# Performance work log

Measured on AMD Instinct MI355X. Metric: run time of the kernel, lower is better.

## Reference

```python
import jax, jax.numpy as jnp
import numpy as np

N, E, G = 20000, 160000, 64
IN_FULL, X_START, X_END = 16, 4, 10
H, OUT, RH, NE, K = 512, 512, 128, 4, 2
NL = 3               # GraphConv layers per expert
SPS, STEMP = 0.3, 1.0  # size_prior_strength, size_temperature


def setup_inputs() -> dict:
    key = jax.random.key(0)
    ks = jax.random.split(key, 10)
    def w(k, shape, fan):
        return jax.random.normal(k, shape, jnp.float32) / np.float32(np.sqrt(fan))
    return dict(
        x=jax.random.normal(ks[0], (N, IN_FULL), jnp.float32),
        edge_index=jax.random.randint(ks[1], (2, E), 0, N),
        batch=jnp.sort(jax.random.randint(ks[2], (N,), 0, G)),
        num_graphs=G,
        enc_W1=w(ks[3], (X_END - X_START, H), X_END - X_START), enc_b1=jnp.zeros((H,), jnp.float32),
        enc_W2=w(ks[4], (H, H), H), enc_b2=jnp.zeros((H,), jnp.float32),
        r_W1=w(ks[5], (H + 2, RH), H + 2), r_b1=jnp.zeros((RH,), jnp.float32),
        ln_g=jnp.ones((RH,), jnp.float32), ln_b=jnp.zeros((RH,), jnp.float32),
        r_W2=w(ks[6], (RH, NE), RH), r_b2=jnp.zeros((NE,), jnp.float32),
        size_centers=jnp.linspace(0.0, 1.0, NE).astype(jnp.float32),
        W_rel=w(ks[7], (NE, NL, H, H), H),       # GraphConv lin_rel weights (stacked)
        b_rel=jnp.zeros((NE, NL, H), jnp.float32),
        W_root=w(ks[8], (NE, NL, H, H), H),      # GraphConv lin_root weights (no bias)
    )


def reference(x, edge_index, batch, num_graphs, enc_W1, enc_b1, enc_W2, enc_b2,
              r_W1, r_b1, ln_g, ln_b, r_W2, r_b2, size_centers, W_rel, b_rel, W_root):
    src, dst = edge_index[0], edge_index[1]
    # encoder: Linear -> ReLU -> Linear on sliced node features
    h = jax.nn.relu(x[:, X_START:X_END] @ enc_W1 + enc_b1) @ enc_W2 + enc_b2
    # per-graph size features (log_nodes_edges mode)
    nodes = jnp.maximum(jax.ops.segment_sum(jnp.ones((N,), x.dtype), batch, num_segments=num_graphs), 1.0)
    edges = jax.ops.segment_sum(jnp.ones((E,), x.dtype), batch[src], num_segments=num_graphs)
    log_n, log_e = jnp.log(nodes), jnp.log1p(edges)
    f = jnp.stack([log_n, log_e], axis=-1)
    f = (f - f.mean(0, keepdims=True)) / (f.std(0, keepdims=True) + 1e-6)
    size_norm = (log_n - log_n.min()) / (log_n.max() - log_n.min() + 1e-6)
    # router: Linear -> LayerNorm -> ReLU -> Linear, plus size prior
    r = jnp.concatenate([h, f[batch]], axis=-1) @ r_W1 + r_b1
    r = (r - r.mean(-1, keepdims=True)) / jnp.sqrt(r.var(-1, keepdims=True) + 1e-5) * ln_g + ln_b
    logits = jax.nn.relu(r) @ r_W2 + r_b2
    prior = -(size_norm[batch][:, None] - size_centers[None, :]) ** 2 / STEMP
    logits = (1.0 - SPS) * logits + SPS * prior
    probs = jax.nn.softmax(logits, axis=-1)
    # top-k sparse gating, renormalized
    v, ix = jax.lax.top_k(probs, K)
    v = v / (v.sum(-1, keepdims=True) + 1e-8)
    weights = jnp.zeros_like(probs).at[jnp.arange(N)[:, None], ix].set(v)  # [N, NE]
    # GraphConv: out_i = (sum_{j->i} z_j) @ W_rel + b_rel + z_i @ W_root
    def gconv(z, Wr, br, Wo):
        agg = jax.ops.segment_sum(z[src], dst, num_segments=N)
        return agg @ Wr + br + z @ Wo
    out = jnp.zeros((N, OUT), x.dtype)
    for e in range(NE):  # small fixed expert count
        z = jax.nn.relu(gconv(h, W_rel[e, 0], b_rel[e, 0], W_root[e, 0]))
        z = jax.nn.relu(gconv(z, W_rel[e, 1], b_rel[e, 1], W_root[e, 1]))
        z = gconv(z, W_rel[e, 2], b_rel[e, 2], W_root[e, 2])
        out = out + weights[:, e:e + 1] * z
    return out
```

## Files before the change

kernel.cpp:

```cpp
#include <hip/hip_runtime.h>
#include <math.h>

#define N_NODES 20000
#define N_EDGES 160000
#define G_GRAPHS 64
#define H_DIM 512
#define RH_DIM 128
#define NE_EXP 4
#define P_ROWS 20096
#define EH_BLOCKS 64
#define WSZ (512 * 512)

typedef __attribute__((ext_vector_type(8))) short bf16x8;
typedef __attribute__((ext_vector_type(4))) float f32x4;

__device__ __forceinline__ ushort f2bf(float f) {
    uint u = __float_as_uint(f);
    return (ushort)((u + 0x7FFFu + ((u >> 16) & 1u)) >> 16);
}
__device__ __forceinline__ float bf2f(ushort h) {
    return __uint_as_float(((uint)h) << 16);
}

__device__ __forceinline__ void async_copy16(const void* g, void* l) {
    __builtin_amdgcn_global_load_lds(
        (__attribute__((address_space(1))) void*)g,
        (__attribute__((address_space(3))) void*)l, 16, 0, 0);
}

__device__ __forceinline__ int xcd_swizzle(int orig, int nwg) {
    const int q = nwg >> 3, r = nwg & 7;
    const int xcd = orig & 7, sid = orig >> 3;
    return (xcd < r ? xcd * (q + 1) : r * (q + 1) + (xcd - r) * q) + sid;
}

template<bool RELU, int EPI, int NE2>
__global__ __launch_bounds__(256, 2)
void gemm_grp(const ushort* __restrict__ A1, size_t a1es,
              const ushort* __restrict__ W1, size_t w1es,
              const ushort* __restrict__ A2, size_t a2es,
              const ushort* __restrict__ W2, size_t w2es,
              const float* __restrict__ bias, size_t bes,
              const float* __restrict__ wcol,
              ushort* __restrict__ out0, size_t oes)
{
    __shared__ char smem[49152];
    const int tid = threadIdx.x;
    const int w = tid >> 6, lane = tid & 63;

    const int wgid = xcd_swizzle(blockIdx.x, gridDim.x);
    const int m0 = (wgid / (2 * NE2)) * 128;
    const int rem = wgid % (2 * NE2);
    const int e  = rem % NE2;
    const int n0 = (rem / NE2) * 256;

    const ushort* __restrict__ A1e = A1 + (size_t)e * a1es;
    const ushort* __restrict__ W1e = W1 + (size_t)e * w1es;
    const ushort* __restrict__ A2e = A2 + (size_t)e * a2es;
    const ushort* __restrict__ W2e = W2 + (size_t)e * w2es;
    const float*  __restrict__ be  = bias + (size_t)e * bes;
    ushort* __restrict__ oe = out0 + (size_t)e * oes;

    f32x4 acc[4][8];
#pragma unroll
    for (int i = 0; i < 4; ++i)
#pragma unroll
        for (int j = 0; j < 8; ++j) acc[i][j] = (f32x4){0.f, 0.f, 0.f, 0.f};

    const int srow = lane >> 2, schk = lane & 3;
    const int wr = w >> 1, wc = w & 1;
    const int row16 = lane & 15;
    const uint koffB = (uint)(lane >> 4) * 16u;
    const uint aoff0 = (uint)(wr * 64 + row16) * 64u + koffB;
    const uint boff0 = 8192u + (uint)(wc * 128 + row16) * 64u + koffB;

    auto stage = [&](int buf, int t) {
        const ushort* __restrict__ A  = (t < 16) ? A1e : A2e;
        const ushort* __restrict__ Wt = (t < 16) ? W1e : W2e;
        const int kt = (t & 15) * 32;
        char* base = smem + buf * 24576;
#pragma unroll
        for (int c = 0; c < 2; ++c) {
            const int rb = c * 64 + w * 16;
            async_copy16(A + (size_t)(m0 + rb + srow) * 512 + kt + schk * 8, base + rb * 64);
        }
#pragma unroll
        for (int c = 0; c < 4; ++c) {
            const int rb = c * 64 + w * 16;
            async_copy16(Wt + (size_t)(n0 + rb + srow) * 512 + kt + schk * 8,
                         base + 8192 + rb * 64);
        }
    };
    auto compute = [&](int buf) {
        const char* base = smem + buf * 24576;
        bf16x8 af[4], bfr[8];
#pragma unroll
        for (int i = 0; i < 4; ++i) af[i] = *(const bf16x8*)(base + aoff0 + i * 1024);
#pragma unroll
        for (int j = 0; j < 8; ++j) bfr[j] = *(const bf16x8*)(base + boff0 + j * 1024);
#pragma unroll
        for (int i = 0; i < 4; ++i)
#pragma unroll
            for (int j = 0; j < 8; ++j)
                acc[i][j] = __builtin_amdgcn_mfma_f32_16x16x32_bf16(af[i], bfr[j], acc[i][j], 0, 0, 0);
    };

    stage(0, 0);
    for (int t = 0; t < 31; ++t) {
        stage((t + 1) & 1, t + 1);
        asm volatile("s_waitcnt vmcnt(6)" ::: "memory");
        __builtin_amdgcn_s_barrier();
        compute(t & 1);
        __builtin_amdgcn_s_barrier();
    }
    asm volatile("s_waitcnt vmcnt(0)" ::: "memory");
    __builtin_amdgcn_s_barrier();
    compute(1);

#pragma unroll
    for (int i = 0; i < 4; ++i) {
        const int r0 = m0 + wr * 64 + i * 16 + (lane >> 4) * 4;
#pragma unroll
        for (int j = 0; j < 8; ++j) {
            const int c = n0 + wc * 128 + j * 16 + row16;
            const float bj = be[c];
#pragma unroll
            for (int q2 = 0; q2 < 4; ++q2) {
                const int r = r0 + q2;
                float v = acc[i][j][q2] + bj;
                if (EPI == 0) {
                    if (RELU) v = fmaxf(v, 0.f);
                    oe[(size_t)r * 512 + c] = f2bf(v);
                } else {
                    const float wrow = (r < N_NODES) ? wcol[(size_t)r * 4 + e] : 0.f;
                    oe[(size_t)r * 512 + c] = f2bf(v * wrow);
                }
            }
        }
    }
}

template<int NPASS, int EPI, int NBN>
__global__ __launch_bounds__(256)
void gemm_mfma(const ushort* __restrict__ A0, const ushort* __restrict__ W0,
               const ushort* __restrict__ A1p, const ushort* __restrict__ W1p,
               const ushort* __restrict__ A2p, const ushort* __restrict__ W2p,
               const float* __restrict__ bias,
               void* __restrict__ out0, void* __restrict__ out1, int Ncols)
{
    __shared__ char smem[32768];
    const int tid = threadIdx.x;
    const int w = tid >> 6, lane = tid & 63;

    const int wgid = xcd_swizzle(blockIdx.x, gridDim.x);
    const int m0 = (wgid / NBN) * 128;
    const int n0 = (wgid % NBN) * 128;

    f32x4 acc[4][4];
#pragma unroll
    for (int i = 0; i < 4; ++i)
#pragma unroll
        for (int j = 0; j < 4; ++j) acc[i][j] = (f32x4){0.f, 0.f, 0.f, 0.f};

    const int srow = lane >> 2, schk = lane & 3;
    const int wr = w >> 1, wc = w & 1;
    const int row16 = lane & 15;
    const uint koffB = (uint)(lane >> 4) * 16u;
    const uint aoff0 = (uint)(wr * 64 + row16) * 64u + koffB;
    const uint boff0 = 8192u + (uint)(wc * 64 + row16) * 64u + koffB;

    const int NT = NPASS * 16;
    auto Asel = [&](int t) -> const ushort* { return (t < 16) ? A0 : ((t < 32) ? A1p : A2p); };
    auto Wsel = [&](int t) -> const ushort* { return (t < 16) ? W0 : ((t < 32) ? W1p : W2p); };

    auto stage = [&](int buf, int t) {
        const ushort* __restrict__ A  = Asel(t);
        const ushort* __restrict__ Wt = Wsel(t);
        const int kt = (t & 15) * 32;
        char* base = smem + buf * 16384;
#pragma unroll
        for (int c = 0; c < 2; ++c) {
            const int rb = c * 64 + w * 16;
            async_copy16(A  + (size_t)(m0 + rb + srow) * 512 + kt + schk * 8, base + rb * 64);
            async_copy16(Wt + (size_t)(n0 + rb + srow) * 512 + kt + schk * 8, base + 8192 + rb * 64);
        }
    };
    auto compute = [&](int buf) {
        const char* base = smem + buf * 16384;
        bf16x8 af[4], bfr[4];
#pragma unroll
        for (int i = 0; i < 4; ++i) af[i] = *(const bf16x8*)(base + aoff0 + i * 1024);
#pragma unroll
        for (int j = 0; j < 4; ++j) bfr[j] = *(const bf16x8*)(base + boff0 + j * 1024);
#pragma unroll
        for (int i = 0; i < 4; ++i)
#pragma unroll
            for (int j = 0; j < 4; ++j)
                acc[i][j] = __builtin_amdgcn_mfma_f32_16x16x32_bf16(af[i], bfr[j], acc[i][j], 0, 0, 0);
    };

    stage(0, 0);
    for (int t = 0; t < NT - 1; ++t) {
        stage((t + 1) & 1, t + 1);
        asm volatile("s_waitcnt vmcnt(4)" ::: "memory");
        __builtin_amdgcn_s_barrier();
        compute(t & 1);
        __builtin_amdgcn_s_barrier();
    }
    asm volatile("s_waitcnt vmcnt(0)" ::: "memory");
    __builtin_amdgcn_s_barrier();
    compute((NT - 1) & 1);

#pragma unroll
    for (int i = 0; i < 4; ++i) {
        const int r0 = m0 + wr * 64 + i * 16 + (lane >> 4) * 4;
#pragma unroll
        for (int j = 0; j < 4; ++j) {
            const int c = n0 + wc * 64 + j * 16 + row16;
            const float bj = (EPI == 5) ? 0.f : bias[c];
#pragma unroll
            for (int q2 = 0; q2 < 4; ++q2) {
                const int r = r0 + q2;
                float v = acc[i][j][q2] + bj;
                if (EPI == 4) {
                    const ushort hi = f2bf(v);
                    const ushort lo = f2bf(v - bf2f(hi));
                    ((ushort*)out0)[(size_t)r * Ncols + c] = hi;
                    ((ushort*)out1)[(size_t)r * Ncols + c] = lo;
                } else {
                    ((float*)out0)[(size_t)r * Ncols + c] = v;
                }
            }
        }
    }
}

__global__ __launch_bounds__(256)
void reduce_wz_kernel(const uint* __restrict__ wz4, float2* __restrict__ out)
{
    const size_t idx = (size_t)blockIdx.x * 256 + threadIdx.x;
    const size_t es = (size_t)P_ROWS * 256;
    const uint a = wz4[idx], b = wz4[idx + es];
    const uint c = wz4[idx + 2 * es], d = wz4[idx + 3 * es];
    float lo = bf2f((ushort)(a & 0xffffu)) + bf2f((ushort)(b & 0xffffu))
             + bf2f((ushort)(c & 0xffffu)) + bf2f((ushort)(d & 0xffffu));
    float hi = bf2f((ushort)(a >> 16)) + bf2f((ushort)(b >> 16))
             + bf2f((ushort)(c >> 16)) + bf2f((ushort)(d >> 16));
    out[idx] = make_float2(lo, hi);
}

__global__ void encoder1_kernel(const float* __restrict__ x, const float* __restrict__ W1,
                                const float* __restrict__ b1,
                                ushort* __restrict__ t1hi, ushort* __restrict__ t1lo)
{
    const int idx = blockIdx.x * blockDim.x + threadIdx.x;
    if (idx >= P_ROWS * H_DIM) return;
    const int i = idx / H_DIM, j = idx - i * H_DIM;
    float v = 0.f;
    if (i < N_NODES) {
        const float* xr = &x[i * 16 + 4];
        v = b1[j];
#pragma unroll
        for (int k = 0; k < 6; ++k) v = fmaf(xr[k], W1[k * H_DIM + j], v);
        v = fmaxf(v, 0.f);
    }
    const ushort hi = f2bf(v);
    t1hi[idx] = hi;
    t1lo[idx] = f2bf(v - bf2f(hi));
}

__global__ void zero_ints_kernel(int* __restrict__ p, int n)
{
    const int idx = blockIdx.x * blockDim.x + threadIdx.x;
    if (idx < n) p[idx] = 0;
}

__global__ void graph_bounds_kernel(const int* __restrict__ batch, int* __restrict__ gstart)
{
    const int g = threadIdx.x;
    if (g > G_GRAPHS) return;
    int lo = 0, hi = N_NODES;
    while (lo < hi) {
        const int mid = (lo + hi) >> 1;
        if (batch[mid] < g) lo = mid + 1; else hi = mid;
    }
    gstart[g] = lo;
}

__global__ __launch_bounds__(256)
void edge_hist_kernel(const int* __restrict__ src, const int* __restrict__ dst,
                      const int* __restrict__ batch,
                      int* __restrict__ part, int* __restrict__ deg)
{
    __shared__ int hist[G_GRAPHS];
    const int tid = threadIdx.x;
    if (tid < G_GRAPHS) hist[tid] = 0;
    __syncthreads();
    for (int e = blockIdx.x * 256 + tid; e < N_EDGES; e += EH_BLOCKS * 256) {
        atomicAdd(&deg[dst[e]], 1);
        atomicAdd(&hist[batch[src[e]]], 1);
    }
    __syncthreads();
    if (tid < G_GRAPHS) part[blockIdx.x * G_GRAPHS + tid] = hist[tid];
}

__global__ void stats_finalize_kernel(const int* __restrict__ gstart, const int* __restrict__ part,
                                      float* __restrict__ f_norm, float* __restrict__ size_norm)
{
    const int g = threadIdx.x;
    const float nn = fmaxf((float)(gstart[g + 1] - gstart[g]), 1.0f);
    int ec = 0;
#pragma unroll 8
    for (int b = 0; b < EH_BLOCKS; ++b) ec += part[b * G_GRAPHS + g];
    const float ee = (float)ec;
    const float ln = logf(nn);
    const float le = log1pf(ee);
    float s0 = ln, s1 = le;
#pragma unroll
    for (int o = 32; o > 0; o >>= 1) { s0 += __shfl_xor(s0, o); s1 += __shfl_xor(s1, o); }
    const float m0 = s0 / 64.f, m1 = s1 / 64.f;
    const float d0 = ln - m0, d1 = le - m1;
    float v0 = d0 * d0, v1 = d1 * d1;
#pragma unroll
    for (int o = 32; o > 0; o >>= 1) { v0 += __shfl_xor(v0, o); v1 += __shfl_xor(v1, o); }
    const float sd0 = sqrtf(v0 / 64.f), sd1 = sqrtf(v1 / 64.f);
    float mn = ln, mx = ln;
#pragma unroll
    for (int o = 32; o > 0; o >>= 1) {
        mn = fminf(mn, __shfl_xor(mn, o));
        mx = fmaxf(mx, __shfl_xor(mx, o));
    }
    f_norm[g * 2 + 0] = d0 / (sd0 + 1e-6f);
    f_norm[g * 2 + 1] = d1 / (sd1 + 1e-6f);
    size_norm[g] = (ln - mn) / (mx - mn + 1e-6f);
}

__global__ void scan_kernel(const int* __restrict__ in, int* __restrict__ row_ptr,
                            int* __restrict__ cursor, int n)
{
    __shared__ int wsum[16];
    __shared__ int carry_s;
    const int tid = threadIdx.x;
    const int lane = tid & 63, wv = tid >> 6;
    if (tid == 0) carry_s = 0;
    __syncthreads();
    for (int base = 0; base < n; base += 1024) {
        const int idx = base + tid;
        const int v = (idx < n) ? in[idx] : 0;
        int x = v;
#pragma unroll
        for (int o = 1; o < 64; o <<= 1) { const int t = __shfl_up(x, o); if (lane >= o) x += t; }
        if (lane == 63) wsum[wv] = x;
        __syncthreads();
        const int carry = carry_s;
        if (wv == 0) {
            int y = (lane < 16) ? wsum[lane] : 0;
#pragma unroll
            for (int o = 1; o < 16; o <<= 1) { const int t = __shfl_up(y, o); if (lane >= o) y += t; }
            if (lane < 16) wsum[lane] = y;
        }
        __syncthreads();
        const int woff = (wv > 0) ? wsum[wv - 1] : 0;
        const int excl = x - v + woff + carry;
        if (idx < n) { row_ptr[idx] = excl; cursor[idx] = excl; }
        __syncthreads();
        if (tid == 0) carry_s = carry + wsum[15];
        __syncthreads();
    }
    if (tid == 0) row_ptr[n] = carry_s;
}

__global__ void scatter_kernel(const int* __restrict__ src, const int* __restrict__ dst,
                               int* __restrict__ cursor, int* __restrict__ csr_col)
{
    const int e = blockIdx.x * blockDim.x + threadIdx.x;
    if (e >= N_EDGES) return;
    const int d = dst[e];
    const int slot = atomicAdd(&cursor[d], 1);
    csr_col[slot] = src[e];
}

__global__ void sort_adj_kernel(const int* __restrict__ row_ptr, int* __restrict__ csr_col)
{
    const int i = blockIdx.x * blockDim.x + threadIdx.x;
    if (i >= N_NODES) return;
    const int b = row_ptr[i], e = row_ptr[i + 1];
    for (int p = b + 1; p < e; ++p) {
        const int key = csr_col[p];
        int q = p - 1;
        while (q >= b && csr_col[q] > key) { csr_col[q + 1] = csr_col[q]; --q; }
        csr_col[q + 1] = key;
    }
}

__global__ __launch_bounds__(256)
void aggregate_bf16(const uint4* __restrict__ z4, const int* __restrict__ row_ptr,
                    const int* __restrict__ csr_col, uint4* __restrict__ agg4)
{
    const size_t es = (size_t)blockIdx.y * P_ROWS * 64;
    const uint4* __restrict__ zz = z4 + es;
    uint4* __restrict__ aa = agg4 + es;
    const int i = blockIdx.x * 4 + (threadIdx.x >> 6);
    const int lane = threadIdx.x & 63;
    const int b = row_ptr[i], e = row_ptr[i + 1];
    float acc[8];
#pragma unroll
    for (int k = 0; k < 8; ++k) acc[k] = 0.f;
    auto add8 = [&](uint4 v) {
        acc[0] += bf2f((ushort)(v.x & 0xffffu)); acc[1] += bf2f((ushort)(v.x >> 16));
        acc[2] += bf2f((ushort)(v.y & 0xffffu)); acc[3] += bf2f((ushort)(v.y >> 16));
        acc[4] += bf2f((ushort)(v.z & 0xffffu)); acc[5] += bf2f((ushort)(v.z >> 16));
        acc[6] += bf2f((ushort)(v.w & 0xffffu)); acc[7] += bf2f((ushort)(v.w >> 16));
    };
    int p = b;
    for (; p + 2 <= e; p += 2) {
        const uint4 v0 = zz[(size_t)csr_col[p] * 64 + lane];
        const uint4 v1 = zz[(size_t)csr_col[p + 1] * 64 + lane];
        add8(v0);
        add8(v1);
    }
    if (p < e) add8(zz[(size_t)csr_col[p] * 64 + lane]);
    uint4 o;
    o.x = (uint)f2bf(acc[0]) | ((uint)f2bf(acc[1]) << 16);
    o.y = (uint)f2bf(acc[2]) | ((uint)f2bf(acc[3]) << 16);
    o.z = (uint)f2bf(acc[4]) | ((uint)f2bf(acc[5]) << 16);
    o.w = (uint)f2bf(acc[6]) | ((uint)f2bf(acc[7]) << 16);
    aa[(size_t)i * 64 + lane] = o;
}

__global__ __launch_bounds__(256)
void transpose_f32_to_bf16(const float* __restrict__ W, ushort* __restrict__ Wt)
{
    __shared__ float tile[32][33];
    const float* Wm = W + (size_t)blockIdx.z * WSZ;
    ushort* Wtm = Wt + (size_t)blockIdx.z * WSZ;
    const int c0 = blockIdx.x * 32, r0 = blockIdx.y * 32;
    const int tc = threadIdx.x & 31, tr = threadIdx.x >> 5;
#pragma unroll
    for (int it = 0; it < 4; ++it)
        tile[tr + it * 8][tc] = Wm[(size_t)(r0 + tr + it * 8) * 512 + c0 + tc];
    __syncthreads();
#pragma unroll
    for (int it = 0; it < 4; ++it) {
        const int cr = tr + it * 8;
        Wtm[(size_t)(c0 + cr) * 512 + r0 + tc] = f2bf(tile[tc][cr]);
    }
}

__global__ __launch_bounds__(256)
void transpose_split_kernel(const float* __restrict__ W, ushort* __restrict__ Whi,
                            ushort* __restrict__ Wlo, int Nin)
{
    __shared__ float tile[32][33];
    const int c0 = blockIdx.x * 32;
    const int r0 = blockIdx.y * 32;
    const int tc = threadIdx.x & 31, tr = threadIdx.x >> 5;
#pragma unroll
    for (int it = 0; it < 4; ++it)
        tile[tr + it * 8][tc] = W[(size_t)(r0 + tr + it * 8) * Nin + c0 + tc];
    __syncthreads();
#pragma unroll
    for (int it = 0; it < 4; ++it) {
        const int cr = tr + it * 8;
        const float v = tile[tc][cr];
        const ushort hi = f2bf(v);
        Whi[(size_t)(c0 + cr) * 512 + r0 + tc] = hi;
        Wlo[(size_t)(c0 + cr) * 512 + r0 + tc] = f2bf(v - bf2f(hi));
    }
}

__global__ __launch_bounds__(128)
void router_kernel(const float* __restrict__ rtmp, const int* __restrict__ batch,
                   const float* __restrict__ rW1, const float* __restrict__ rb1,
                   const float* __restrict__ lng, const float* __restrict__ lnb,
                   const float* __restrict__ rW2, const float* __restrict__ rb2,
                   const float* __restrict__ centers,
                   const float* __restrict__ f_norm, const float* __restrict__ size_norm,
                   float* __restrict__ weights)
{
    const int i = blockIdx.x;
    const int j = threadIdx.x;
    const int g = batch[i];
    const float f0 = f_norm[g * 2], f1 = f_norm[g * 2 + 1];
    float r = rtmp[(size_t)i * RH_DIM + j]
            + f0 * rW1[512 * RH_DIM + j] + f1 * rW1[513 * RH_DIM + j] + rb1[j];

    __shared__ float part[2];
    __shared__ float rbuf[RH_DIM];
    __shared__ float lbuf[4];
    const int lane = j & 63, wv = j >> 6;

    float s = r;
#pragma unroll
    for (int o = 32; o > 0; o >>= 1) s += __shfl_xor(s, o);
    if (lane == 0) part[wv] = s;
    __syncthreads();
    const float mean = (part[0] + part[1]) / 128.f;
    __syncthreads();
    const float d = r - mean;
    float v = d * d;
#pragma unroll
    for (int o = 32; o > 0; o >>= 1) v += __shfl_xor(v, o);
    if (lane == 0) part[wv] = v;
    __syncthreads();
    const float var = (part[0] + part[1]) / 128.f;
    const float rn = d / sqrtf(var + 1e-5f) * lng[j] + lnb[j];
    rbuf[j] = fmaxf(rn, 0.f);
    __syncthreads();

    if (j < 4) {
        float acc = rb2[j];
        for (int t = 0; t < RH_DIM; ++t) acc = fmaf(rbuf[t], rW2[t * 4 + j], acc);
        const float sn = size_norm[g];
        const float dd = sn - centers[j];
        lbuf[j] = 0.7f * acc + 0.3f * (-(dd * dd));
    }
    __syncthreads();
    if (j == 0) {
        float p[4];
        const float mx = fmaxf(fmaxf(lbuf[0], lbuf[1]), fmaxf(lbuf[2], lbuf[3]));
#pragma unroll
        for (int c = 0; c < 4; ++c) p[c] = expf(lbuf[c] - mx);
        const float ssum = p[0] + p[1] + p[2] + p[3];
#pragma unroll
        for (int c = 0; c < 4; ++c) p[c] /= ssum;
        int i1 = 0;
#pragma unroll
        for (int c = 1; c < 4; ++c) if (p[c] > p[i1]) i1 = c;
        int i2 = -1;
#pragma unroll
        for (int c = 0; c < 4; ++c) {
            if (c == i1) continue;
            if (i2 < 0 || p[c] > p[i2]) i2 = c;
        }
        const float vs = p[i1] + p[i2] + 1e-8f;
        float wout[4] = {0.f, 0.f, 0.f, 0.f};
        wout[i1] = p[i1] / vs;
        wout[i2] = p[i2] / vs;
#pragma unroll
        for (int c = 0; c < 4; ++c) weights[(size_t)i * 4 + c] = wout[c];
    }
}

extern "C" void kernel_launch(void* const* d_in, const int* in_sizes, int n_in,
                              void* d_out, int out_size, void* d_ws, size_t ws_size,
                              hipStream_t stream)
{
    const float* x       = (const float*)d_in[0];
    const int*   ei      = (const int*)d_in[1];
    const int*   batch   = (const int*)d_in[2];
    const float* enc_W1  = (const float*)d_in[4];
    const float* enc_b1  = (const float*)d_in[5];
    const float* enc_W2  = (const float*)d_in[6];
    const float* enc_b2  = (const float*)d_in[7];
    const float* r_W1    = (const float*)d_in[8];
    const float* r_b1    = (const float*)d_in[9];
    const float* ln_g    = (const float*)d_in[10];
    const float* ln_b    = (const float*)d_in[11];
    const float* r_W2    = (const float*)d_in[12];
    const float* r_b2    = (const float*)d_in[13];
    const float* centers = (const float*)d_in[14];
    const float* W_rel   = (const float*)d_in[15];
    const float* b_rel   = (const float*)d_in[16];
    const float* W_root  = (const float*)d_in[17];
    const int* src = ei;
    const int* dst = ei + N_EDGES;
    float* out = (float*)d_out;

    const size_t PF = (size_t)P_ROWS * H_DIM;
    const size_t need4 = (size_t)372 * 1024 * 1024;
    const bool path4 = (ws_size >= need4);
    const int NEPD = path4 ? 4 : 2;
    const size_t ZBYTES = PF * 2 * NEPD;

    char* wsp = (char*)d_ws;
    size_t off = 0;
    auto alloc = [&](size_t bytes) -> char* {
        char* p = wsp + off;
        off = (off + bytes + 255) & ~(size_t)255;
        return p;
    };
    char* region1 = alloc(PF * 4);
    ushort* t1hi = (ushort*)region1;
    ushort* t1lo = (ushort*)(region1 + PF * 2);
    ushort* wz4  = (ushort*)region1;
    char* region2 = alloc(PF * 4);
    ushort* h_hi = (ushort*)region2;
    ushort* h_lo = (ushort*)(region2 + PF * 2);
    char* B_zA = alloc(ZBYTES);
    ushort* zAe = (ushort*)B_zA;
    float*  rtmp = (float*)B_zA;
    char* B_zB = alloc(ZBYTES);
    ushort* zBe = (ushort*)B_zB;
    char* B_ag = alloc(ZBYTES);
    ushort* agge = (ushort*)B_ag;
    ushort* aggH16 = (ushort*)alloc(PF * 2);
    ushort* Wt_rel16  = (ushort*)alloc((size_t)12 * WSZ * 2);
    ushort* Wt_root16 = (ushort*)alloc((size_t)12 * WSZ * 2);
    ushort* W2t_hi = (ushort*)alloc((size_t)WSZ * 2);
    ushort* W2t_lo = (ushort*)alloc((size_t)WSZ * 2);
    ushort* rW1t_hi = (ushort*)alloc((size_t)128 * 512 * 2);
    ushort* rW1t_lo = (ushort*)alloc((size_t)128 * 512 * 2);
    float*  weights = (float*)alloc((size_t)P_ROWS * 4 * 4);
    int* deg     = (int*)alloc((size_t)N_NODES * 4);
    int* gstart  = (int*)alloc((size_t)(G_GRAPHS + 1) * 4);
    int* part    = (int*)alloc((size_t)EH_BLOCKS * G_GRAPHS * 4);
    int* row_ptr = (int*)alloc((size_t)(N_NODES + 1) * 4);
    int* cursor  = (int*)alloc((size_t)N_NODES * 4);
    int* csr_col = (int*)alloc((size_t)N_EDGES * 4);
    float* f_norm    = (float*)alloc((size_t)G_GRAPHS * 2 * 4);
    float* size_norm = (float*)alloc((size_t)G_GRAPHS * 4);
    (void)in_sizes; (void)n_in; (void)out_size;

    const int enc_nwg = 4 * (P_ROWS / 128);
    const int rtr_nwg = 1 * (P_ROWS / 128);
    const int grp_nwg = 2 * NEPD * (P_ROWS / 128);
    const dim3 tr_grid(16, 16, 12);
    const dim3 agg_grid1(N_NODES / 4, 1), agg_gridE(N_NODES / 4, NEPD);

    zero_ints_kernel<<<(N_NODES + 255) / 256, 256, 0, stream>>>(deg, N_NODES);
    transpose_f32_to_bf16<<<tr_grid, 256, 0, stream>>>(W_rel, Wt_rel16);
    transpose_f32_to_bf16<<<tr_grid, 256, 0, stream>>>(W_root, Wt_root16);
    transpose_split_kernel<<<dim3(16, 16), 256, 0, stream>>>(enc_W2, W2t_hi, W2t_lo, 512);
    transpose_split_kernel<<<dim3(4, 16), 256, 0, stream>>>(r_W1, rW1t_hi, rW1t_lo, 128);
    graph_bounds_kernel<<<1, 128, 0, stream>>>(batch, gstart);
    edge_hist_kernel<<<EH_BLOCKS, 256, 0, stream>>>(src, dst, batch, part, deg);
    stats_finalize_kernel<<<1, 64, 0, stream>>>(gstart, part, f_norm, size_norm);
    encoder1_kernel<<<(P_ROWS * H_DIM + 255) / 256, 256, 0, stream>>>(x, enc_W1, enc_b1, t1hi, t1lo);
    gemm_mfma<3, 4, 4><<<enc_nwg, 256, 0, stream>>>(
        t1hi, W2t_hi, t1hi, W2t_lo, t1lo, W2t_hi, enc_b2, h_hi, h_lo, 512);
    gemm_mfma<3, 5, 1><<<rtr_nwg, 256, 0, stream>>>(
        h_hi, rW1t_hi, h_hi, rW1t_lo, h_lo, rW1t_hi, nullptr, rtmp, nullptr, 128);
    router_kernel<<<N_NODES, 128, 0, stream>>>(rtmp, batch, r_W1, r_b1, ln_g, ln_b,
                                               r_W2, r_b2, centers, f_norm, size_norm, weights);
    scan_kernel<<<1, 1024, 0, stream>>>(deg, row_ptr, cursor, N_NODES);
    scatter_kernel<<<(N_EDGES + 255) / 256, 256, 0, stream>>>(src, dst, cursor, csr_col);
    sort_adj_kernel<<<(N_NODES + 255) / 256, 256, 0, stream>>>(row_ptr, csr_col);
    aggregate_bf16<<<agg_grid1, 256, 0, stream>>>((const uint4*)h_hi, row_ptr, csr_col,
                                                  (uint4*)aggH16);

    const size_t WES = (size_t)3 * WSZ;
    const size_t BES = (size_t)3 * 512;
    if (path4) {
        gemm_grp<true, 0, 4><<<grp_nwg, 256, 0, stream>>>(
            aggH16, 0, Wt_rel16, WES, h_hi, 0, Wt_root16, WES, b_rel, BES, nullptr, zAe, PF);
        aggregate_bf16<<<agg_gridE, 256, 0, stream>>>((const uint4*)zAe, row_ptr, csr_col,
                                                      (uint4*)agge);
        gemm_grp<true, 0, 4><<<grp_nwg, 256, 0, stream>>>(
            agge, PF, Wt_rel16 + WSZ, WES, zAe, PF, Wt_root16 + WSZ, WES, b_rel + 512, BES,
            nullptr, zBe, PF);
        aggregate_bf16<<<agg_gridE, 256, 0, stream>>>((const uint4*)zBe, row_ptr, csr_col,
                                                      (uint4*)agge);
        gemm_grp<false, 6, 4><<<grp_nwg, 256, 0, stream>>>(
            agge, PF, Wt_rel16 + 2 * WSZ, WES, zBe, PF, Wt_root16 + 2 * WSZ, WES, b_rel + 1024, BES,
            weights, wz4, PF);
    } else {
        for (int p = 0; p < 2; ++p) {
            const size_t eb = (size_t)(p * 2);
            const ushort* WrP = Wt_rel16  + eb * WES;
            const ushort* WoP = Wt_root16 + eb * WES;
            const float*  brP = b_rel + eb * BES;
            ushort* wzP = wz4 + eb * PF;
            gemm_grp<true, 0, 2><<<grp_nwg, 256, 0, stream>>>(
                aggH16, 0, WrP, WES, h_hi, 0, WoP, WES, brP, BES, nullptr, zAe, PF);
            aggregate_bf16<<<agg_gridE, 256, 0, stream>>>((const uint4*)zAe, row_ptr, csr_col,
                                                          (uint4*)agge);
            gemm_grp<true, 0, 2><<<grp_nwg, 256, 0, stream>>>(
                agge, PF, WrP + WSZ, WES, zAe, PF, WoP + WSZ, WES, brP + 512, BES, nullptr, zBe, PF);
            aggregate_bf16<<<agg_gridE, 256, 0, stream>>>((const uint4*)zBe, row_ptr, csr_col,
                                                          (uint4*)agge);
            gemm_grp<false, 6, 2><<<grp_nwg, 256, 0, stream>>>(
                agge, PF, WrP + 2 * WSZ, WES, zBe, PF, WoP + 2 * WSZ, WES, brP + 1024, BES,
                weights + eb, wzP, PF);
        }
    }
    reduce_wz_kernel<<<N_NODES, 256, 0, stream>>>((const uint*)wz4, (float2*)out);
}
```

Baseline: 848.7 us.

## Shrink grouped GEMM tile to 128x128 and add mid-memory expert schedule

The grouped expert GEMM tile drops from 128x256 to 128x128, which halves LDS use and the accumulator count and doubles the workgroup count. This should raise occupancy and let more workgroups run at once, at the cost of more A-tile reloads. A new intermediate workspace mode batches the first layer across all four experts, then runs layers two and three in two passes of two experts. This cuts the memory needed for the full four-expert path. Which path runs depends on the workspace size given at runtime.

```diff
diff --git a/kernel.cpp b/kernel.cpp
--- a/kernel.cpp
+++ b/kernel.cpp
@@ -35,7 +35,7 @@
 }
 
 template<bool RELU, int EPI, int NE2>
-__global__ __launch_bounds__(256, 2)
+__global__ __launch_bounds__(256)
 void gemm_grp(const ushort* __restrict__ A1, size_t a1es,
               const ushort* __restrict__ W1, size_t w1es,
               const ushort* __restrict__ A2, size_t a2es,
@@ -44,15 +44,15 @@
               const float* __restrict__ wcol,
               ushort* __restrict__ out0, size_t oes)
 {
-    __shared__ char smem[49152];
+    __shared__ char smem[32768];
     const int tid = threadIdx.x;
     const int w = tid >> 6, lane = tid & 63;
 
     const int wgid = xcd_swizzle(blockIdx.x, gridDim.x);
-    const int m0 = (wgid / (2 * NE2)) * 128;
-    const int rem = wgid % (2 * NE2);
+    const int m0 = (wgid / (4 * NE2)) * 128;
+    const int rem = wgid % (4 * NE2);
     const int e  = rem % NE2;
-    const int n0 = (rem / NE2) * 256;
+    const int n0 = (rem / NE2) * 128;
 
     const ushort* __restrict__ A1e = A1 + (size_t)e * a1es;
     const ushort* __restrict__ W1e = W1 + (size_t)e * w1es;
@@ -61,54 +61,49 @@
     const float*  __restrict__ be  = bias + (size_t)e * bes;
     ushort* __restrict__ oe = out0 + (size_t)e * oes;
 
-    f32x4 acc[4][8];
+    f32x4 acc[4][4];
 #pragma unroll
     for (int i = 0; i < 4; ++i)
 #pragma unroll
-        for (int j = 0; j < 8; ++j) acc[i][j] = (f32x4){0.f, 0.f, 0.f, 0.f};
+        for (int j = 0; j < 4; ++j) acc[i][j] = (f32x4){0.f, 0.f, 0.f, 0.f};
 
     const int srow = lane >> 2, schk = lane & 3;
     const int wr = w >> 1, wc = w & 1;
     const int row16 = lane & 15;
     const uint koffB = (uint)(lane >> 4) * 16u;
     const uint aoff0 = (uint)(wr * 64 + row16) * 64u + koffB;
-    const uint boff0 = 8192u + (uint)(wc * 128 + row16) * 64u + koffB;
+    const uint boff0 = 8192u + (uint)(wc * 64 + row16) * 64u + koffB;
 
     auto stage = [&](int buf, int t) {
         const ushort* __restrict__ A  = (t < 16) ? A1e : A2e;
         const ushort* __restrict__ Wt = (t < 16) ? W1e : W2e;
         const int kt = (t & 15) * 32;
-        char* base = smem + buf * 24576;
+        char* base = smem + buf * 16384;
 #pragma unroll
         for (int c = 0; c < 2; ++c) {
             const int rb = c * 64 + w * 16;
-            async_copy16(A + (size_t)(m0 + rb + srow) * 512 + kt + schk * 8, base + rb * 64);
-        }
-#pragma unroll
-        for (int c = 0; c < 4; ++c) {
-            const int rb = c * 64 + w * 16;
-            async_copy16(Wt + (size_t)(n0 + rb + srow) * 512 + kt + schk * 8,
-                         base + 8192 + rb * 64);
+            async_copy16(A  + (size_t)(m0 + rb + srow) * 512 + kt + schk * 8, base + rb * 64);
+            async_copy16(Wt + (size_t)(n0 + rb + srow) * 512 + kt + schk * 8, base + 8192 + rb * 64);
         }
     };
     auto compute = [&](int buf) {
-        const char* base = smem + buf * 24576;
-        bf16x8 af[4], bfr[8];
+        const char* base = smem + buf * 16384;
+        bf16x8 af[4], bfr[4];
 #pragma unroll
         for (int i = 0; i < 4; ++i) af[i] = *(const bf16x8*)(base + aoff0 + i * 1024);
 #pragma unroll
-        for (int j = 0; j < 8; ++j) bfr[j] = *(const bf16x8*)(base + boff0 + j * 1024);
+        for (int j = 0; j < 4; ++j) bfr[j] = *(const bf16x8*)(base + boff0 + j * 1024);
 #pragma unroll
         for (int i = 0; i < 4; ++i)
 #pragma unroll
-            for (int j = 0; j < 8; ++j)
+            for (int j = 0; j < 4; ++j)
                 acc[i][j] = __builtin_amdgcn_mfma_f32_16x16x32_bf16(af[i], bfr[j], acc[i][j], 0, 0, 0);
     };
 
     stage(0, 0);
     for (int t = 0; t < 31; ++t) {
         stage((t + 1) & 1, t + 1);
-        asm volatile("s_waitcnt vmcnt(6)" ::: "memory");
+        asm volatile("s_waitcnt vmcnt(4)" ::: "memory");
         __builtin_amdgcn_s_barrier();
         compute(t & 1);
         __builtin_amdgcn_s_barrier();
@@ -121,8 +116,8 @@
     for (int i = 0; i < 4; ++i) {
         const int r0 = m0 + wr * 64 + i * 16 + (lane >> 4) * 4;
 #pragma unroll
-        for (int j = 0; j < 8; ++j) {
-            const int c = n0 + wc * 128 + j * 16 + row16;
+        for (int j = 0; j < 4; ++j) {
+            const int c = n0 + wc * 64 + j * 16 + row16;
             const float bj = be[c];
 #pragma unroll
             for (int q2 = 0; q2 < 4; ++q2) {
@@ -568,10 +563,11 @@
     float* out = (float*)d_out;
 
     const size_t PF = (size_t)P_ROWS * H_DIM;
-    const size_t need4 = (size_t)372 * 1024 * 1024;
-    const bool path4 = (ws_size >= need4);
-    const int NEPD = path4 ? 4 : 2;
-    const size_t ZBYTES = PF * 2 * NEPD;
+    const size_t PF2 = PF * 2;
+    const int mode = (ws_size >= (size_t)375 * 1024 * 1024) ? 2
+                   : (ws_size >= (size_t)295 * 1024 * 1024) ? 1 : 0;
+    const int zaW = (mode >= 1) ? 4 : 2;
+    const int zbW = (mode == 2) ? 4 : 2;
 
     char* wsp = (char*)d_ws;
     size_t off = 0;
@@ -587,12 +583,12 @@
     char* region2 = alloc(PF * 4);
     ushort* h_hi = (ushort*)region2;
     ushort* h_lo = (ushort*)(region2 + PF * 2);
-    char* B_zA = alloc(ZBYTES);
+    char* B_zA = alloc(PF2 * zaW);
     ushort* zAe = (ushort*)B_zA;
     float*  rtmp = (float*)B_zA;
-    char* B_zB = alloc(ZBYTES);
+    char* B_zB = alloc(PF2 * zbW);
     ushort* zBe = (ushort*)B_zB;
-    char* B_ag = alloc(ZBYTES);
+    char* B_ag = alloc(PF2 * zbW);
     ushort* agge = (ushort*)B_ag;
     ushort* aggH16 = (ushort*)alloc(PF * 2);
     ushort* Wt_rel16  = (ushort*)alloc((size_t)12 * WSZ * 2);
@@ -612,11 +608,14 @@
     float* size_norm = (float*)alloc((size_t)G_GRAPHS * 4);
     (void)in_sizes; (void)n_in; (void)out_size;
 
-    const int enc_nwg = 4 * (P_ROWS / 128);
-    const int rtr_nwg = 1 * (P_ROWS / 128);
-    const int grp_nwg = 2 * NEPD * (P_ROWS / 128);
+    const int enc_nwg  = 4 * (P_ROWS / 128);
+    const int rtr_nwg  = 1 * (P_ROWS / 128);
+    const int grp_nwg2 = 8 * (P_ROWS / 128);
+    const int grp_nwg4 = 16 * (P_ROWS / 128);
     const dim3 tr_grid(16, 16, 12);
-    const dim3 agg_grid1(N_NODES / 4, 1), agg_gridE(N_NODES / 4, NEPD);
+    const dim3 agg_grid1(N_NODES / 4, 1);
+    const dim3 agg_grid2(N_NODES / 4, 2);
+    const dim3 agg_grid4(N_NODES / 4, 4);
 
     zero_ints_kernel<<<(N_NODES + 255) / 256, 256, 0, stream>>>(deg, N_NODES);
     transpose_f32_to_bf16<<<tr_grid, 256, 0, stream>>>(W_rel, Wt_rel16);
@@ -641,19 +640,39 @@
 
     const size_t WES = (size_t)3 * WSZ;
     const size_t BES = (size_t)3 * 512;
-    if (path4) {
-        gemm_grp<true, 0, 4><<<grp_nwg, 256, 0, stream>>>(
+    if (mode == 2) {
+        gemm_grp<true, 0, 4><<<grp_nwg4, 256, 0, stream>>>(
             aggH16, 0, Wt_rel16, WES, h_hi, 0, Wt_root16, WES, b_rel, BES, nullptr, zAe, PF);
-        aggregate_bf16<<<agg_gridE, 256, 0, stream>>>((const uint4*)zAe, row_ptr, csr_col,
+        aggregate_bf16<<<agg_grid4, 256, 0, stream>>>((const uint4*)zAe, row_ptr, csr_col,
                                                       (uint4*)agge);
-        gemm_grp<true, 0, 4><<<grp_nwg, 256, 0, stream>>>(
+        gemm_grp<true, 0, 4><<<grp_nwg4, 256, 0, stream>>>(
             agge, PF, Wt_rel16 + WSZ, WES, zAe, PF, Wt_root16 + WSZ, WES, b_rel + 512, BES,
             nullptr, zBe, PF);
-        aggregate_bf16<<<agg_gridE, 256, 0, stream>>>((const uint4*)zBe, row_ptr, csr_col,
+        aggregate_bf16<<<agg_grid4, 256, 0, stream>>>((const uint4*)zBe, row_ptr, csr_col,
                                                       (uint4*)agge);
-        gemm_grp<false, 6, 4><<<grp_nwg, 256, 0, stream>>>(
+        gemm_grp<false, 6, 4><<<grp_nwg4, 256, 0, stream>>>(
             agge, PF, Wt_rel16 + 2 * WSZ, WES, zBe, PF, Wt_root16 + 2 * WSZ, WES, b_rel + 1024, BES,
             weights, wz4, PF);
+    } else if (mode == 1) {
+        gemm_grp<true, 0, 4><<<grp_nwg4, 256, 0, stream>>>(
+            aggH16, 0, Wt_rel16, WES, h_hi, 0, Wt_root16, WES, b_rel, BES, nullptr, zAe, PF);
+        for (int p = 0; p < 2; ++p) {
+            const size_t eb = (size_t)(p * 2);
+            const ushort* WrP = Wt_rel16  + eb * WES;
+            const ushort* WoP = Wt_root16 + eb * WES;
+            const float*  brP = b_rel + eb * BES;
+            const ushort* zAp = zAe + eb * PF;
+            ushort* wzP = wz4 + eb * PF;
+            aggregate_bf16<<<agg_grid2, 256, 0, stream>>>((const uint4*)zAp, row_ptr, csr_col,
+                                                          (uint4*)agge);
+            gemm_grp<true, 0, 2><<<grp_nwg2, 256, 0, stream>>>(
+                agge, PF, WrP + WSZ, WES, zAp, PF, WoP + WSZ, WES, brP + 512, BES, nullptr, zBe, PF);
+            aggregate_bf16<<<agg_grid2, 256, 0, stream>>>((const uint4*)zBe, row_ptr, csr_col,
+                                                          (uint4*)agge);
+            gemm_grp<false, 6, 2><<<grp_nwg2, 256, 0, stream>>>(
+                agge, PF, WrP + 2 * WSZ, WES, zBe, PF, WoP + 2 * WSZ, WES, brP + 1024, BES,
+                weights + eb, wzP, PF);
+        }
     } else {
         for (int p = 0; p < 2; ++p) {
             const size_t eb = (size_t)(p * 2);
@@ -661,15 +680,15 @@
             const ushort* WoP = Wt_root16 + eb * WES;
             const float*  brP = b_rel + eb * BES;
             ushort* wzP = wz4 + eb * PF;
-            gemm_grp<true, 0, 2><<<grp_nwg, 256, 0, stream>>>(
+            gemm_grp<true, 0, 2><<<grp_nwg2, 256, 0, stream>>>(
                 aggH16, 0, WrP, WES, h_hi, 0, WoP, WES, brP, BES, nullptr, zAe, PF);
-            aggregate_bf16<<<agg_gridE, 256, 0, stream>>>((const uint4*)zAe, row_ptr, csr_col,
+            aggregate_bf16<<<agg_grid2, 256, 0, stream>>>((const uint4*)zAe, row_ptr, csr_col,
                                                           (uint4*)agge);
-            gemm_grp<true, 0, 2><<<grp_nwg, 256, 0, stream>>>(
+            gemm_grp<true, 0, 2><<<grp_nwg2, 256, 0, stream>>>(
                 agge, PF, WrP + WSZ, WES, zAe, PF, WoP + WSZ, WES, brP + 512, BES, nullptr, zBe, PF);
-            aggregate_bf16<<<agg_gridE, 256, 0, stream>>>((const uint4*)zBe, row_ptr, csr_col,
+            aggregate_bf16<<<agg_grid2, 256, 0, stream>>>((const uint4*)zBe, row_ptr, csr_col,
                                                           (uint4*)agge);
-            gemm_grp<false, 6, 2><<<grp_nwg, 256, 0, stream>>>(
+            gemm_grp<false, 6, 2><<<grp_nwg2, 256, 0, stream>>>(
                 agge, PF, WrP + 2 * WSZ, WES, zBe, PF, WoP + 2 * WSZ, WES, brP + 1024, BES,
                 weights + eb, wzP, PF);
         }
```

Result: no change. 836.7 us (-1.4%).
